# Kernel optimization log

Hardware: AMD Instinct MI355X
Metric: run time of the kernel (lower is better)

Reference implementation:

```python
import jax, jax.numpy as jnp
import numpy as np

C_IN, C_OUT, K, DG, PAD = 256, 256, 3, 2, 1
EPS = 1e-5


def setup_inputs() -> dict:
    key = jax.random.key(0)
    k = jax.random.split(key, 8)
    B, H, W = 4, 64, 64
    x = jax.random.normal(k[0], (B, C_IN, H, W), jnp.float32)
    # offset/mask conv (DCNv2 pack): 3 * dg * k * k output channels
    w_off = jax.random.normal(k[1], (3 * DG * K * K, C_IN, K, K), jnp.float32) * 0.01
    b_off = jnp.zeros((3 * DG * K * K,), jnp.float32)
    # main deformable conv weight
    w = jax.random.normal(k[2], (C_OUT, C_IN, K, K), jnp.float32) * (1.0 / np.sqrt(C_IN * K * K))
    b = jnp.zeros((C_OUT,), jnp.float32)
    # BatchNorm (eval mode: running stats)
    gamma = jnp.ones((C_OUT,), jnp.float32)
    beta = jnp.zeros((C_OUT,), jnp.float32)
    running_mean = jax.random.normal(k[3], (C_OUT,), jnp.float32) * 0.1
    running_var = jax.random.uniform(k[4], (C_OUT,), jnp.float32, 0.5, 1.5)
    return dict(x=x, w_off=w_off, b_off=b_off, w=w, b=b, gamma=gamma, beta=beta,
                running_mean=running_mean, running_var=running_var)


def _conv2d_same(x, w, b):
    y = jax.lax.conv_general_dilated(x, w, (1, 1), 'SAME',
                                     dimension_numbers=('NCHW', 'OIHW', 'NCHW'))
    return y + b[None, :, None, None]


def _deform_conv(x, w_off, b_off, w, b):
    B, C, H, W = x.shape
    K2 = K * K
    Cg = C // DG
    # offsets + modulation mask from internal conv (DCNv2 pack)
    om = _conv2d_same(x, w_off, b_off)            # [B, 3*DG*K2, H, W]
    o1, o2, m = jnp.split(om, 3, axis=1)
    mask = jax.nn.sigmoid(m).reshape(B, DG, 1, K2, H * W)
    off_y = o1.reshape(B, DG, K2, H, W)
    off_x = o2.reshape(B, DG, K2, H, W)
    # base sampling grid: output pixel + kernel tap - pad
    ki = jnp.arange(K)
    ky = (jnp.repeat(ki, K) - PAD).astype(jnp.float32)   # [K2]
    kx = (jnp.tile(ki, K) - PAD).astype(jnp.float32)     # [K2]
    py = off_y + ky[:, None, None] + jnp.arange(H, dtype=jnp.float32)[None, :, None]
    px = off_x + kx[:, None, None] + jnp.arange(W, dtype=jnp.float32)[None, None, :]
    y0 = jnp.floor(py)
    x0 = jnp.floor(px)
    ly = (py - y0).reshape(B, DG, 1, K2, H * W)
    lx = (px - x0).reshape(B, DG, 1, K2, H * W)
    y0i = y0.astype(jnp.int32)
    x0i = x0.astype(jnp.int32)
    xg = x.reshape(B, DG, Cg, H * W)

    def gather(yi, xi):
        # zero-padded bilinear corner gather, per deformable group
        valid = (yi >= 0) & (yi < H) & (xi >= 0) & (xi < W)
        lin = jnp.clip(yi, 0, H - 1) * W + jnp.clip(xi, 0, W - 1)
        v = jnp.take_along_axis(xg[:, :, :, None, :],
                                lin.reshape(B, DG, 1, K2, H * W), axis=-1)
        return v * valid.reshape(B, DG, 1, K2, H * W)

    val = (gather(y0i, x0i) * (1 - ly) * (1 - lx)
           + gather(y0i, x0i + 1) * (1 - ly) * lx
           + gather(y0i + 1, x0i) * ly * (1 - lx)
           + gather(y0i + 1, x0i + 1) * ly * lx)
    val = val * mask                               # [B, DG, Cg, K2, H*W]
    wr = w.reshape(C_OUT, DG, Cg, K2)
    out = jnp.einsum('bgckn,ogck->bon', val, wr).reshape(B, C_OUT, H, W)
    return out + b[None, :, None, None]


def reference(x, w_off, b_off, w, b, gamma, beta, running_mean, running_var):
    y = _deform_conv(x, w_off, b_off, w, b)
    inv = gamma / jnp.sqrt(running_var + EPS)
    y = (y - running_mean[None, :, None, None]) * inv[None, :, None, None] + beta[None, :, None, None]
    return jax.nn.relu(y)
```

## Files before the change

kernel.cpp:

```cpp
#include <hip/hip_runtime.h>
#include <math.h>

typedef __bf16 bf16x8 __attribute__((ext_vector_type(8)));
typedef __bf16 bf16x4 __attribute__((ext_vector_type(4)));
typedef __bf16 bf16x2 __attribute__((ext_vector_type(2)));
typedef float  f32x4  __attribute__((ext_vector_type(4)));

#define MFMA16(a, b, c) __builtin_amdgcn_mfma_f32_16x16x32_bf16((a), (b), (c), 0, 0, 0)

__global__ __launch_bounds__(256) void xpose_kernel(
    const float* __restrict__ x, __bf16* __restrict__ xT) {
  __shared__ float xs[64][65];
  int t = threadIdx.x;
  int b = blockIdx.x >> 6, y = blockIdx.x & 63;
  for (int cc = 0; cc < 4; ++cc) {
    __syncthreads();
    for (int i = t; i < 4096; i += 256) {
      int cl = i >> 6, xc = i & 63;
      xs[cl][xc] = x[(((size_t)b * 256 + cc * 64 + cl) * 64 + y) * 64 + xc];
    }
    __syncthreads();
    for (int i = t; i < 4096; i += 256) {
      int xc = i >> 6, cl = i & 63;
      xT[(((size_t)b * 64 + y) * 64 + xc) * 256 + cc * 64 + cl] = (__bf16)xs[cl][xc];
    }
  }
}

__global__ __launch_bounds__(256) void prep_kernel(
    const float* __restrict__ w, const float* __restrict__ w_off,
    const float* __restrict__ bconv, const float* __restrict__ gamma,
    const float* __restrict__ beta, const float* __restrict__ mean,
    const float* __restrict__ var,
    __bf16* __restrict__ wFragD, __bf16* __restrict__ wFragO,
    float* __restrict__ sc, float* __restrict__ sh) {
  int i = blockIdx.x * 256 + threadIdx.x;
  if (i < 589824) {
    int j = i & 7, lane = (i >> 3) & 63, ocb = (i >> 9) & 15;
    int kc = (i >> 13) & 3, gk = i >> 15;
    int klocal = (lane >> 4) * 8 + j;
    int oc = ocb * 16 + (lane & 15);
    int c = kc * 32 + klocal;
    int g = gk / 9, ktap = gk % 9;
    wFragD[i] = (__bf16)w[((size_t)oc * 256 + g * 128 + c) * 9 + ktap];
  } else {
    int i2 = i - 589824;
    int j = i2 & 7, lane = (i2 >> 3) & 63, ocb = (i2 >> 9) & 3;
    int kc = (i2 >> 11) & 7, tap = i2 >> 14;
    int klocal = (lane >> 4) * 8 + j;
    int oc = ocb * 16 + (lane & 15);
    int ci = kc * 32 + klocal;
    wFragO[i2] = (oc < 54) ? (__bf16)w_off[((size_t)oc * 256 + ci) * 9 + tap]
                           : (__bf16)0.f;
  }
  if (i < 256) {
    float s = gamma[i] * rsqrtf(var[i] + 1e-5f);
    sc[i] = s;
    sh[i] = (bconv[i] - mean[i]) * s + beta[i];
  }
}

__global__ __launch_bounds__(512) void offconv_kernel(
    const __bf16* __restrict__ xT, const __bf16* __restrict__ wFragO,
    const float* __restrict__ b_off, float* __restrict__ om) {
  __shared__ __attribute__((aligned(16))) __bf16 atile[2][64 * 264];
  int t = threadIdx.x;
  int b = blockIdx.x >> 6, y = blockIdx.x & 63;
  int lane = t & 63, wv = t >> 6;
  int l15 = lane & 15, quad = lane >> 4;
  int mh = wv & 1, ocq = wv >> 1;
  const __bf16* xTb = xT + (size_t)b * 64 * 64 * 256;

  f32x4 acc0 = {0.f, 0.f, 0.f, 0.f};
  f32x4 acc1 = {0.f, 0.f, 0.f, 0.f};
  const bf16x4 z4 = {(__bf16)0.f, (__bf16)0.f, (__bf16)0.f, (__bf16)0.f};

  {
    int y2 = y - 1;
    #pragma unroll
    for (int pp = 0; pp < 8; ++pp) {
      int p = wv * 8 + pp, x2 = p - 1;
      bool inb = (y2 >= 0) && (x2 >= 0);
      bf16x4 v = inb ? *(const bf16x4*)(xTb + (((size_t)y2 * 64 + x2) * 256) + 4 * lane)
                     : z4;
      *(bf16x4*)&atile[0][p * 264 + 4 * lane] = v;
    }
  }

  for (int tap = 0; tap < 9; ++tap) {
    __syncthreads();
    bf16x4 g[8];
    bool inb[8];
    if (tap < 8) {
      int dy = (tap + 1) / 3 - 1, dx = (tap + 1) % 3 - 1;
      int y2 = y + dy;
      #pragma unroll
      for (int pp = 0; pp < 8; ++pp) {
        int p = wv * 8 + pp, x2 = p + dx;
        inb[pp] = (y2 >= 0) && (y2 < 64) && (x2 >= 0) && (x2 < 64);
        int cy = inb[pp] ? y2 : 0, cx = inb[pp] ? x2 : 0;
        g[pp] = *(const bf16x4*)(xTb + (((size_t)cy * 64 + cx) * 256) + 4 * lane);
      }
    }
    const __bf16* arow = atile[tap & 1] + (mh * 32 + l15) * 264 + quad * 8;
    const __bf16* bbase = wFragO + ((size_t)(tap * 8) * 4 + ocq) * 512 + lane * 8;
    #pragma unroll
    for (int kc = 0; kc < 8; ++kc) {
      bf16x8 bf = *(const bf16x8*)(bbase + (size_t)kc * 4 * 512);
      bf16x8 a0 = *(const bf16x8*)(arow + kc * 32);
      bf16x8 a1 = *(const bf16x8*)(arow + 16 * 264 + kc * 32);
      acc0 = MFMA16(a0, bf, acc0);
      acc1 = MFMA16(a1, bf, acc1);
    }
    if (tap < 8) {
      __bf16* dst = atile[(tap + 1) & 1];
      #pragma unroll
      for (int pp = 0; pp < 8; ++pp) {
        bf16x4 v = inb[pp] ? g[pp] : z4;
        *(bf16x4*)&dst[(wv * 8 + pp) * 264 + 4 * lane] = v;
      }
    }
  }

  int oc = ocq * 16 + l15;
  if (oc < 54) {
    float bo = b_off[oc];
    #pragma unroll
    for (int fm = 0; fm < 2; ++fm) {
      f32x4 v = fm ? acc1 : acc0;
      f32x4 r = {v.x + bo, v.y + bo, v.z + bo, v.w + bo};
      int pxs = mh * 32 + fm * 16 + quad * 4;
      *(f32x4*)(om + (((size_t)b * 54 + oc) * 64 + y) * 64 + pxs) = r;
    }
  }
}

__global__ __launch_bounds__(512) void dconv_kernel(
    const __bf16* __restrict__ xT, const float* __restrict__ om,
    const __bf16* __restrict__ wFragD, const float* __restrict__ sc,
    const float* __restrict__ sh, float* __restrict__ out) {
  __shared__ float swgt[18 * 64 * 4];
  __shared__ int   slin[18 * 64 * 4];
  __shared__ __attribute__((aligned(16))) __bf16 atile[2][64 * 136];
  int t = threadIdx.x;
  int b = blockIdx.x >> 6, y = blockIdx.x & 63;
  int lane = t & 63, wv = t >> 6;
  int l15 = lane & 15, quad = lane >> 4;
  const __bf16* xTb = xT + (size_t)b * 64 * 64 * 256;

  for (int i = t; i < 18 * 64; i += 512) {
    int gk = i >> 6, p = i & 63;
    int k = gk % 9;
    size_t obase = (size_t)b * 54 * 4096 + (size_t)y * 64 + p;
    float oy = om[obase + (size_t)gk * 4096];
    float ox = om[obase + (size_t)(18 + gk) * 4096];
    float mz = om[obase + (size_t)(36 + gk) * 4096];
    float mv = 1.f / (1.f + expf(-mz));
    float py  = (float)(y + (k / 3) - 1) + oy;
    float pxf = (float)(p + (k % 3) - 1) + ox;
    float y0f = floorf(py), x0f = floorf(pxf);
    int y0 = (int)y0f, x0 = (int)x0f;
    float ly = py - y0f, lx = pxf - x0f;
    int y1 = y0 + 1, x1 = x0 + 1;
    bool vy0 = (y0 >= 0) && (y0 < 64), vy1 = (y1 >= 0) && (y1 < 64);
    bool vx0 = (x0 >= 0) && (x0 < 64), vx1 = (x1 >= 0) && (x1 < 64);
    int cy0 = min(max(y0, 0), 63), cy1 = min(max(y1, 0), 63);
    int cx0 = min(max(x0, 0), 63), cx1 = min(max(x1, 0), 63);
    swgt[i * 4 + 0] = (vy0 && vx0) ? (1.f - ly) * (1.f - lx) * mv : 0.f;
    swgt[i * 4 + 1] = (vy0 && vx1) ? (1.f - ly) * lx * mv : 0.f;
    swgt[i * 4 + 2] = (vy1 && vx0) ? ly * (1.f - lx) * mv : 0.f;
    swgt[i * 4 + 3] = (vy1 && vx1) ? ly * lx * mv : 0.f;
    slin[i * 4 + 0] = (cy0 * 64 + cx0) * 256;
    slin[i * 4 + 1] = (cy0 * 64 + cx1) * 256;
    slin[i * 4 + 2] = (cy1 * 64 + cx0) * 256;
    slin[i * 4 + 3] = (cy1 * 64 + cx1) * 256;
  }

  f32x4 acc[4][2];
  #pragma unroll
  for (int fm = 0; fm < 4; ++fm)
    #pragma unroll
    for (int fn = 0; fn < 2; ++fn)
      acc[fm][fn] = (f32x4){0.f, 0.f, 0.f, 0.f};

  __syncthreads();

  {
    const __bf16* xg = xTb + 2 * lane;
    #pragma unroll
    for (int pp = 0; pp < 8; ++pp) {
      int p = wv * 8 + pp, base = p * 4;
      float v0 = 0.f, v1 = 0.f;
      #pragma unroll
      for (int i = 0; i < 4; ++i) {
        float s = swgt[base + i];
        bf16x2 vv = *(const bf16x2*)(xg + slin[base + i]);
        v0 += s * (float)vv.x;
        v1 += s * (float)vv.y;
      }
      bf16x2 o = {(__bf16)v0, (__bf16)v1};
      *(bf16x2*)&atile[0][p * 136 + 2 * lane] = o;
    }
  }

  for (int gk = 0; gk < 18; ++gk) {
    __syncthreads();
    bf16x2 gv[8][4];
    float gs[8][4];
    if (gk < 17) {
      int gn = gk + 1;
      const __bf16* xg = xTb + (gn / 9) * 128 + 2 * lane;
      #pragma unroll
      for (int pp = 0; pp < 8; ++pp) {
        int p = wv * 8 + pp, base = (gn * 64 + p) * 4;
        #pragma unroll
        for (int i = 0; i < 4; ++i) {
          gs[pp][i] = swgt[base + i];
          gv[pp][i] = *(const bf16x2*)(xg + slin[base + i]);
        }
      }
    }
    const __bf16* arow = atile[gk & 1] + l15 * 136 + quad * 8;
    const __bf16* bbase = wFragD + ((size_t)(gk * 4) * 16 + wv * 2) * 512 + lane * 8;
    #pragma unroll
    for (int kc = 0; kc < 4; ++kc) {
      bf16x8 b0 = *(const bf16x8*)(bbase + (size_t)kc * 16 * 512);
      bf16x8 b1 = *(const bf16x8*)(bbase + (size_t)kc * 16 * 512 + 512);
      #pragma unroll
      for (int fm = 0; fm < 4; ++fm) {
        bf16x8 a = *(const bf16x8*)(arow + fm * 16 * 136 + kc * 32);
        acc[fm][0] = MFMA16(a, b0, acc[fm][0]);
        acc[fm][1] = MFMA16(a, b1, acc[fm][1]);
      }
    }
    if (gk < 17) {
      __bf16* dst = atile[(gk + 1) & 1];
      #pragma unroll
      for (int pp = 0; pp < 8; ++pp) {
        float v0 = gs[pp][0] * (float)gv[pp][0].x + gs[pp][1] * (float)gv[pp][1].x
                 + gs[pp][2] * (float)gv[pp][2].x + gs[pp][3] * (float)gv[pp][3].x;
        float v1 = gs[pp][0] * (float)gv[pp][0].y + gs[pp][1] * (float)gv[pp][1].y
                 + gs[pp][2] * (float)gv[pp][2].y + gs[pp][3] * (float)gv[pp][3].y;
        bf16x2 o = {(__bf16)v0, (__bf16)v1};
        *(bf16x2*)&dst[(wv * 8 + pp) * 136 + 2 * lane] = o;
      }
    }
  }

  #pragma unroll
  for (int fm = 0; fm < 4; ++fm) {
    #pragma unroll
    for (int fn = 0; fn < 2; ++fn) {
      int oc = wv * 32 + fn * 16 + l15;
      float s = sc[oc], h = sh[oc];
      f32x4 v = acc[fm][fn];
      f32x4 r = {fmaxf(v.x * s + h, 0.f), fmaxf(v.y * s + h, 0.f),
                 fmaxf(v.z * s + h, 0.f), fmaxf(v.w * s + h, 0.f)};
      int pxs = fm * 16 + quad * 4;
      *(f32x4*)(out + (((size_t)b * 256 + oc) * 64 + y) * 64 + pxs) = r;
    }
  }
}

extern "C" void kernel_launch(void* const* d_in, const int* in_sizes, int n_in,
                              void* d_out, int out_size, void* d_ws, size_t ws_size,
                              hipStream_t stream) {
  const float* x     = (const float*)d_in[0];
  const float* w_off = (const float*)d_in[1];
  const float* b_off = (const float*)d_in[2];
  const float* w     = (const float*)d_in[3];
  const float* bconv = (const float*)d_in[4];
  const float* gamma = (const float*)d_in[5];
  const float* beta  = (const float*)d_in[6];
  const float* rmean = (const float*)d_in[7];
  const float* rvar  = (const float*)d_in[8];
  float* out = (float*)d_out;

  float*  om     = (float*)d_ws;
  __bf16* xT     = (__bf16*)((char*)d_ws + 3538944);
  __bf16* wFragD = (__bf16*)((char*)d_ws + 11927552);
  __bf16* wFragO = (__bf16*)((char*)d_ws + 13107200);
  float*  sc     = (float*)((char*)d_ws + 13402112);
  float*  sh     = (float*)((char*)d_ws + 13403136);

  xpose_kernel<<<4 * 64, 256, 0, stream>>>(x, xT);
  prep_kernel<<<2880, 256, 0, stream>>>(w, w_off, bconv, gamma, beta, rmean, rvar,
                                        wFragD, wFragO, sc, sh);
  offconv_kernel<<<4 * 64, 512, 0, stream>>>(xT, wFragO, b_off, om);
  dconv_kernel<<<4 * 64, 512, 0, stream>>>(xT, om, wFragD, sc, sh, out);
}
```

Baseline: 148.2 us.

## Restructure offset conv, deformable gather, and transpose for wider loads and reuse

The transpose kernel is split across four times as many blocks, one per 64-channel chunk, for more parallelism. The offset conv now stages three padded input rows once in XOR-swizzled LDS and reads every tap from them, which removes the per-tap global gathers and barriers. The deformable conv gathers 8 bf16 channels per load using vectorized weight/index tables, stores into a swizzled LDS tile, and prefetches the B fragments into registers one step ahead. The costs are higher register and LDS use (rowbuf is about 101KB), which may lower occupancy.

```diff
diff --git a/kernel.cpp b/kernel.cpp
--- a/kernel.cpp
+++ b/kernel.cpp
@@ -2,28 +2,26 @@
 #include <math.h>
 
 typedef __bf16 bf16x8 __attribute__((ext_vector_type(8)));
-typedef __bf16 bf16x4 __attribute__((ext_vector_type(4)));
-typedef __bf16 bf16x2 __attribute__((ext_vector_type(2)));
 typedef float  f32x4  __attribute__((ext_vector_type(4)));
+typedef int    i32x4  __attribute__((ext_vector_type(4)));
 
 #define MFMA16(a, b, c) __builtin_amdgcn_mfma_f32_16x16x32_bf16((a), (b), (c), 0, 0, 0)
+
+#define ATIDX(r, c) ((r) * 128 + (((c) ^ ((r) & 7)) * 8))
 
 __global__ __launch_bounds__(256) void xpose_kernel(
     const float* __restrict__ x, __bf16* __restrict__ xT) {
   __shared__ float xs[64][65];
   int t = threadIdx.x;
-  int b = blockIdx.x >> 6, y = blockIdx.x & 63;
-  for (int cc = 0; cc < 4; ++cc) {
-    __syncthreads();
-    for (int i = t; i < 4096; i += 256) {
-      int cl = i >> 6, xc = i & 63;
-      xs[cl][xc] = x[(((size_t)b * 256 + cc * 64 + cl) * 64 + y) * 64 + xc];
-    }
-    __syncthreads();
-    for (int i = t; i < 4096; i += 256) {
-      int xc = i >> 6, cl = i & 63;
-      xT[(((size_t)b * 64 + y) * 64 + xc) * 256 + cc * 64 + cl] = (__bf16)xs[cl][xc];
-    }
+  int b = blockIdx.x >> 8, y = (blockIdx.x >> 2) & 63, cc = blockIdx.x & 3;
+  for (int i = t; i < 4096; i += 256) {
+    int cl = i >> 6, xc = i & 63;
+    xs[cl][xc] = x[(((size_t)b * 256 + cc * 64 + cl) * 64 + y) * 64 + xc];
+  }
+  __syncthreads();
+  for (int i = t; i < 4096; i += 256) {
+    int xc = i >> 6, cl = i & 63;
+    xT[(((size_t)b * 64 + y) * 64 + xc) * 256 + cc * 64 + cl] = (__bf16)xs[cl][xc];
   }
 }
 
@@ -63,62 +61,45 @@
 __global__ __launch_bounds__(512) void offconv_kernel(
     const __bf16* __restrict__ xT, const __bf16* __restrict__ wFragO,
     const float* __restrict__ b_off, float* __restrict__ om) {
-  __shared__ __attribute__((aligned(16))) __bf16 atile[2][64 * 264];
+  __shared__ __attribute__((aligned(16))) __bf16 rowbuf[3 * 66 * 256];
   int t = threadIdx.x;
   int b = blockIdx.x >> 6, y = blockIdx.x & 63;
   int lane = t & 63, wv = t >> 6;
   int l15 = lane & 15, quad = lane >> 4;
   int mh = wv & 1, ocq = wv >> 1;
   const __bf16* xTb = xT + (size_t)b * 64 * 64 * 256;
+  bf16x8 z8;
+  #pragma unroll
+  for (int e = 0; e < 8; ++e) z8[e] = (__bf16)0.f;
+
+  for (int i = t; i < 3 * 66 * 32; i += 512) {
+    int c = i & 31, px66 = (i >> 5) % 66, dy = i / 2112;
+    int y2 = y + dy - 1, x2 = px66 - 1;
+    bf16x8 v = z8;
+    if (y2 >= 0 && y2 < 64 && x2 >= 0 && x2 < 64)
+      v = *(const bf16x8*)(xTb + ((size_t)y2 * 64 + x2) * 256 + c * 8);
+    *(bf16x8*)&rowbuf[dy * 16896 + px66 * 256 + ((c ^ (px66 & 7)) * 8)] = v;
+  }
+  __syncthreads();
 
   f32x4 acc0 = {0.f, 0.f, 0.f, 0.f};
   f32x4 acc1 = {0.f, 0.f, 0.f, 0.f};
-  const bf16x4 z4 = {(__bf16)0.f, (__bf16)0.f, (__bf16)0.f, (__bf16)0.f};
-
-  {
-    int y2 = y - 1;
-    #pragma unroll
-    for (int pp = 0; pp < 8; ++pp) {
-      int p = wv * 8 + pp, x2 = p - 1;
-      bool inb = (y2 >= 0) && (x2 >= 0);
-      bf16x4 v = inb ? *(const bf16x4*)(xTb + (((size_t)y2 * 64 + x2) * 256) + 4 * lane)
-                     : z4;
-      *(bf16x4*)&atile[0][p * 264 + 4 * lane] = v;
-    }
-  }
-
   for (int tap = 0; tap < 9; ++tap) {
-    __syncthreads();
-    bf16x4 g[8];
-    bool inb[8];
-    if (tap < 8) {
-      int dy = (tap + 1) / 3 - 1, dx = (tap + 1) % 3 - 1;
-      int y2 = y + dy;
-      #pragma unroll
-      for (int pp = 0; pp < 8; ++pp) {
-        int p = wv * 8 + pp, x2 = p + dx;
-        inb[pp] = (y2 >= 0) && (y2 < 64) && (x2 >= 0) && (x2 < 64);
-        int cy = inb[pp] ? y2 : 0, cx = inb[pp] ? x2 : 0;
-        g[pp] = *(const bf16x4*)(xTb + (((size_t)cy * 64 + cx) * 256) + 4 * lane);
-      }
-    }
-    const __bf16* arow = atile[tap & 1] + (mh * 32 + l15) * 264 + quad * 8;
-    const __bf16* bbase = wFragO + ((size_t)(tap * 8) * 4 + ocq) * 512 + lane * 8;
+    int dy = tap / 3, dxs = tap % 3;
+    const __bf16* bb = wFragO + ((size_t)(tap * 8) * 4 + ocq) * 512 + lane * 8;
+    bf16x8 Bf[8];
+    #pragma unroll
+    for (int kc = 0; kc < 8; ++kc)
+      Bf[kc] = *(const bf16x8*)(bb + (size_t)kc * 4 * 512);
+    int p0 = mh * 32 + l15 + dxs, p1 = p0 + 16;
+    const __bf16* rb = rowbuf + dy * 16896;
     #pragma unroll
     for (int kc = 0; kc < 8; ++kc) {
-      bf16x8 bf = *(const bf16x8*)(bbase + (size_t)kc * 4 * 512);
-      bf16x8 a0 = *(const bf16x8*)(arow + kc * 32);
-      bf16x8 a1 = *(const bf16x8*)(arow + 16 * 264 + kc * 32);
-      acc0 = MFMA16(a0, bf, acc0);
-      acc1 = MFMA16(a1, bf, acc1);
-    }
-    if (tap < 8) {
-      __bf16* dst = atile[(tap + 1) & 1];
-      #pragma unroll
-      for (int pp = 0; pp < 8; ++pp) {
-        bf16x4 v = inb[pp] ? g[pp] : z4;
-        *(bf16x4*)&dst[(wv * 8 + pp) * 264 + 4 * lane] = v;
-      }
+      int c = kc * 4 + quad;
+      bf16x8 a0 = *(const bf16x8*)&rb[p0 * 256 + ((c ^ (p0 & 7)) * 8)];
+      bf16x8 a1 = *(const bf16x8*)&rb[p1 * 256 + ((c ^ (p1 & 7)) * 8)];
+      acc0 = MFMA16(a0, Bf[kc], acc0);
+      acc1 = MFMA16(a1, Bf[kc], acc1);
     }
   }
 
@@ -139,9 +120,9 @@
     const __bf16* __restrict__ xT, const float* __restrict__ om,
     const __bf16* __restrict__ wFragD, const float* __restrict__ sc,
     const float* __restrict__ sh, float* __restrict__ out) {
-  __shared__ float swgt[18 * 64 * 4];
-  __shared__ int   slin[18 * 64 * 4];
-  __shared__ __attribute__((aligned(16))) __bf16 atile[2][64 * 136];
+  __shared__ f32x4 swgtv[18 * 64];
+  __shared__ i32x4 slinv[18 * 64];
+  __shared__ __attribute__((aligned(16))) __bf16 atile[2][64 * 128];
   int t = threadIdx.x;
   int b = blockIdx.x >> 6, y = blockIdx.x & 63;
   int lane = t & 63, wv = t >> 6;
@@ -166,14 +147,18 @@
     bool vx0 = (x0 >= 0) && (x0 < 64), vx1 = (x1 >= 0) && (x1 < 64);
     int cy0 = min(max(y0, 0), 63), cy1 = min(max(y1, 0), 63);
     int cx0 = min(max(x0, 0), 63), cx1 = min(max(x1, 0), 63);
-    swgt[i * 4 + 0] = (vy0 && vx0) ? (1.f - ly) * (1.f - lx) * mv : 0.f;
-    swgt[i * 4 + 1] = (vy0 && vx1) ? (1.f - ly) * lx * mv : 0.f;
-    swgt[i * 4 + 2] = (vy1 && vx0) ? ly * (1.f - lx) * mv : 0.f;
-    swgt[i * 4 + 3] = (vy1 && vx1) ? ly * lx * mv : 0.f;
-    slin[i * 4 + 0] = (cy0 * 64 + cx0) * 256;
-    slin[i * 4 + 1] = (cy0 * 64 + cx1) * 256;
-    slin[i * 4 + 2] = (cy1 * 64 + cx0) * 256;
-    slin[i * 4 + 3] = (cy1 * 64 + cx1) * 256;
+    f32x4 sv;
+    sv.x = (vy0 && vx0) ? (1.f - ly) * (1.f - lx) * mv : 0.f;
+    sv.y = (vy0 && vx1) ? (1.f - ly) * lx * mv : 0.f;
+    sv.z = (vy1 && vx0) ? ly * (1.f - lx) * mv : 0.f;
+    sv.w = (vy1 && vx1) ? ly * lx * mv : 0.f;
+    i32x4 lv;
+    lv.x = (cy0 * 64 + cx0) * 256;
+    lv.y = (cy0 * 64 + cx1) * 256;
+    lv.z = (cy1 * 64 + cx0) * 256;
+    lv.w = (cy1 * 64 + cx1) * 256;
+    swgtv[i] = sv;
+    slinv[i] = lv;
   }
 
   f32x4 acc[4][2];
@@ -185,64 +170,82 @@
 
   __syncthreads();
 
+  int ch0 = l15 * 8;
   {
-    const __bf16* xg = xTb + 2 * lane;
-    #pragma unroll
-    for (int pp = 0; pp < 8; ++pp) {
-      int p = wv * 8 + pp, base = p * 4;
-      float v0 = 0.f, v1 = 0.f;
-      #pragma unroll
-      for (int i = 0; i < 4; ++i) {
-        float s = swgt[base + i];
-        bf16x2 vv = *(const bf16x2*)(xg + slin[base + i]);
-        v0 += s * (float)vv.x;
-        v1 += s * (float)vv.y;
-      }
-      bf16x2 o = {(__bf16)v0, (__bf16)v1};
-      *(bf16x2*)&atile[0][p * 136 + 2 * lane] = o;
+    const __bf16* xg = xTb + ch0;
+    #pragma unroll
+    for (int j = 0; j < 2; ++j) {
+      int p = wv * 8 + j * 4 + quad;
+      f32x4 sv = swgtv[p];
+      i32x4 lv = slinv[p];
+      bf16x8 c0 = *(const bf16x8*)(xg + lv.x);
+      bf16x8 c1 = *(const bf16x8*)(xg + lv.y);
+      bf16x8 c2 = *(const bf16x8*)(xg + lv.z);
+      bf16x8 c3 = *(const bf16x8*)(xg + lv.w);
+      bf16x8 o;
+      #pragma unroll
+      for (int e = 0; e < 8; ++e)
+        o[e] = (__bf16)(sv.x * (float)c0[e] + sv.y * (float)c1[e]
+                      + sv.z * (float)c2[e] + sv.w * (float)c3[e]);
+      *(bf16x8*)&atile[0][ATIDX(p, l15)] = o;
+    }
+  }
+  bf16x8 Bf[8];
+  {
+    const __bf16* bb = wFragD + ((size_t)wv * 2) * 512 + lane * 8;
+    #pragma unroll
+    for (int kc = 0; kc < 4; ++kc) {
+      Bf[kc * 2]     = *(const bf16x8*)(bb + (size_t)kc * 16 * 512);
+      Bf[kc * 2 + 1] = *(const bf16x8*)(bb + (size_t)kc * 16 * 512 + 512);
     }
   }
 
   for (int gk = 0; gk < 18; ++gk) {
     __syncthreads();
-    bf16x2 gv[8][4];
-    float gs[8][4];
+    bf16x8 cr[2][4];
+    f32x4 sv[2];
+    int pj[2];
     if (gk < 17) {
       int gn = gk + 1;
-      const __bf16* xg = xTb + (gn / 9) * 128 + 2 * lane;
-      #pragma unroll
-      for (int pp = 0; pp < 8; ++pp) {
-        int p = wv * 8 + pp, base = (gn * 64 + p) * 4;
-        #pragma unroll
-        for (int i = 0; i < 4; ++i) {
-          gs[pp][i] = swgt[base + i];
-          gv[pp][i] = *(const bf16x2*)(xg + slin[base + i]);
-        }
-      }
-    }
-    const __bf16* arow = atile[gk & 1] + l15 * 136 + quad * 8;
-    const __bf16* bbase = wFragD + ((size_t)(gk * 4) * 16 + wv * 2) * 512 + lane * 8;
+      const __bf16* xg = xTb + (gn / 9) * 128 + ch0;
+      #pragma unroll
+      for (int j = 0; j < 2; ++j) {
+        int p = wv * 8 + j * 4 + quad;
+        pj[j] = p;
+        sv[j] = swgtv[gn * 64 + p];
+        i32x4 lv = slinv[gn * 64 + p];
+        cr[j][0] = *(const bf16x8*)(xg + lv.x);
+        cr[j][1] = *(const bf16x8*)(xg + lv.y);
+        cr[j][2] = *(const bf16x8*)(xg + lv.z);
+        cr[j][3] = *(const bf16x8*)(xg + lv.w);
+      }
+    }
+    const __bf16* at = atile[gk & 1];
     #pragma unroll
     for (int kc = 0; kc < 4; ++kc) {
-      bf16x8 b0 = *(const bf16x8*)(bbase + (size_t)kc * 16 * 512);
-      bf16x8 b1 = *(const bf16x8*)(bbase + (size_t)kc * 16 * 512 + 512);
       #pragma unroll
       for (int fm = 0; fm < 4; ++fm) {
-        bf16x8 a = *(const bf16x8*)(arow + fm * 16 * 136 + kc * 32);
-        acc[fm][0] = MFMA16(a, b0, acc[fm][0]);
-        acc[fm][1] = MFMA16(a, b1, acc[fm][1]);
+        bf16x8 a = *(const bf16x8*)&at[ATIDX(fm * 16 + l15, kc * 4 + quad)];
+        acc[fm][0] = MFMA16(a, Bf[kc * 2],     acc[fm][0]);
+        acc[fm][1] = MFMA16(a, Bf[kc * 2 + 1], acc[fm][1]);
       }
     }
     if (gk < 17) {
       __bf16* dst = atile[(gk + 1) & 1];
       #pragma unroll
-      for (int pp = 0; pp < 8; ++pp) {
-        float v0 = gs[pp][0] * (float)gv[pp][0].x + gs[pp][1] * (float)gv[pp][1].x
-                 + gs[pp][2] * (float)gv[pp][2].x + gs[pp][3] * (float)gv[pp][3].x;
-        float v1 = gs[pp][0] * (float)gv[pp][0].y + gs[pp][1] * (float)gv[pp][1].y
-                 + gs[pp][2] * (float)gv[pp][2].y + gs[pp][3] * (float)gv[pp][3].y;
-        bf16x2 o = {(__bf16)v0, (__bf16)v1};
-        *(bf16x2*)&dst[(wv * 8 + pp) * 136 + 2 * lane] = o;
+      for (int j = 0; j < 2; ++j) {
+        bf16x8 o;
+        #pragma unroll
+        for (int e = 0; e < 8; ++e)
+          o[e] = (__bf16)(sv[j].x * (float)cr[j][0][e] + sv[j].y * (float)cr[j][1][e]
+                        + sv[j].z * (float)cr[j][2][e] + sv[j].w * (float)cr[j][3][e]);
+        *(bf16x8*)&dst[ATIDX(pj[j], l15)] = o;
+      }
+      const __bf16* bb = wFragD + ((size_t)((gk + 1) * 4) * 16 + wv * 2) * 512 + lane * 8;
+      #pragma unroll
+      for (int kc = 0; kc < 4; ++kc) {
+        Bf[kc * 2]     = *(const bf16x8*)(bb + (size_t)kc * 16 * 512);
+        Bf[kc * 2 + 1] = *(const bf16x8*)(bb + (size_t)kc * 16 * 512 + 512);
       }
     }
   }
@@ -283,7 +286,7 @@
   float*  sc     = (float*)((char*)d_ws + 13402112);
   float*  sh     = (float*)((char*)d_ws + 13403136);
 
-  xpose_kernel<<<4 * 64, 256, 0, stream>>>(x, xT);
+  xpose_kernel<<<4 * 64 * 4, 256, 0, stream>>>(x, xT);
   prep_kernel<<<2880, 256, 0, stream>>>(w, w_off, bconv, gamma, beta, rmean, rvar,
                                         wFragD, wFragO, sc, sh);
   offconv_kernel<<<4 * 64, 512, 0, stream>>>(xT, wFragO, b_off, om);
```

Result: faster. 138.2 us (-6.8%).
